# Kernel optimization log

Hardware: AMD Instinct MI355X
Metric: run time of the kernel (lower is better)

## Reference

```python
import jax, jax.numpy as jnp
import numpy as np

B, N, S, D = 8, 8192, 4, 256


def setup_inputs() -> dict:
    key = jax.random.key(0)
    kx, kj, kk, k1, k2, k3, k4 = jax.random.split(key, 7)
    x = jax.random.normal(kx, (B, N, D), dtype=jnp.float32)
    ji = jax.random.randint(kj, (B, N, S), 0, N, dtype=jnp.int64)
    ki = jax.random.randint(kk, (B, N, S), 0, N, dtype=jnp.int64)
    # params of nn.Sequential(Linear(3D, D), GELU, Linear(D, D))
    W1 = jax.random.normal(k1, (3 * D, D), dtype=jnp.float32) * 0.02
    b1 = jax.random.normal(k2, (D,), dtype=jnp.float32) * 0.02
    W2 = jax.random.normal(k3, (D, D), dtype=jnp.float32) * 0.02
    b2 = jax.random.normal(k4, (D,), dtype=jnp.float32) * 0.02
    return {"x": x, "ji": ji, "ki": ki, "W1": W1, "b1": b1, "W2": W2, "b2": b2}


def reference(x, ji, ki, W1, b1, W2, b2):
    # gather neighbor features per batch element: [B,N,S,D]
    gather = jax.vmap(lambda xb, ib: xb[ib])
    xj = gather(x, ji)
    xk = gather(x, ki)
    xi = jnp.broadcast_to(x[:, :, None, :], (B, N, S, D))
    h = jnp.concatenate([xi, xj, xk], axis=-1)            # [B,N,S,3D]
    h = jax.nn.gelu(jnp.einsum('bnse,ed->bnsd', h, W1) + b1, approximate=False)
    out = jnp.einsum('bnse,ed->bnsd', h, W2) + b2         # [B,N,S,D]
    return out.mean(axis=2)                               # [B,N,D]
```

## Files before the change

### kernel.cpp

```cpp
#include <hip/hip_runtime.h>
#include <hip/hip_bf16.h>

#define Bb 8
#define Nn 8192
#define Ss 4
#define Dd 256
#define MTOT (Bb*Nn)

typedef unsigned short u16;
typedef short short8 __attribute__((ext_vector_type(8)));
typedef unsigned short u16x4 __attribute__((ext_vector_type(4)));
typedef float f32x4 __attribute__((ext_vector_type(4)));

static __device__ __forceinline__ float bf2f(u16 v) {
  union { unsigned int u; float f; } x; x.u = ((unsigned int)v) << 16; return x.f;
}
static __device__ __forceinline__ u16 f2bf(float f) {
  union { float f; unsigned int u; } x; x.f = f;
  unsigned int u = x.u;
  return (u16)((u + 0x7fffu + ((u >> 16) & 1u)) >> 16);
}

static __device__ __forceinline__ float gelu_fast(float x) {
  float x2 = x * x;
  float z = x * (-2.3021277f - 0.10294456f * x2);
  float e = __builtin_amdgcn_exp2f(z);
  return x * __builtin_amdgcn_rcpf(1.0f + e);
}

__global__ __launch_bounds__(256) void prep_kernel(
    const float* __restrict__ x, const float* __restrict__ W1,
    const float* __restrict__ W2,
    u16* __restrict__ xb, u16* __restrict__ W1t, u16* __restrict__ W2t)
{
  int bid = blockIdx.x, t = threadIdx.x;
  if (bid < 16384) {
    size_t i = ((size_t)bid * 256 + t) * 4;
    f32x4 v = *(const f32x4*)&x[i];
    u16x4 o;
    o[0] = f2bf(v[0]); o[1] = f2bf(v[1]); o[2] = f2bf(v[2]); o[3] = f2bf(v[3]);
    *(u16x4*)&xb[i] = o;
  } else if (bid < 16384 + 768) {
    int j = (bid - 16384) * 256 + t;
    int n = j >> 8, k = j & 255;
    int tb = n >> 8, d = n & 255;
    W1t[j] = f2bf(W1[(size_t)(tb * 256 + k) * 256 + d]);
  } else {
    int j = (bid - 17152) * 256 + t;
    int n = j >> 8, k = j & 255;
    W2t[j] = f2bf(W2[(size_t)k * 256 + n]);
  }
}

template<int MODE>
__global__ __launch_bounds__(256) void gemm128(
    const u16* __restrict__ Ag, const u16* __restrict__ Btg,
    void* __restrict__ Outv, const float* __restrict__ bias, int ldOut)
{
  __shared__ u16 As[128 * 64];
  __shared__ u16 Bs[128 * 64];
  const int t = threadIdx.x;
  const int w = t >> 6, lane = t & 63;
  const int wm = (w >> 1) * 64, wn = (w & 1) * 64;
  const int lr = lane & 15;
  const int lk = (lane >> 4) * 8;
  const size_t m0 = (size_t)blockIdx.x * 128;
  const int n0 = blockIdx.y * 128;

  f32x4 acc[4][4];
#pragma unroll
  for (int m = 0; m < 4; ++m)
#pragma unroll
    for (int n = 0; n < 4; ++n)
      acc[m][n] = (f32x4){0.f, 0.f, 0.f, 0.f};

  for (int kt = 0; kt < 4; ++kt) {
#pragma unroll
    for (int pass = 0; pass < 4; ++pass) {
      int c = pass * 256 + t;
      int row = c >> 3, cc = c & 7;
      const u16* ga = Ag + (m0 + row) * 256 + kt * 64 + cc * 8;
      u16* la = As + pass * 2048 + (t & 192) * 8;
      __builtin_amdgcn_global_load_lds(
          (const __attribute__((address_space(1))) void*)ga,
          (__attribute__((address_space(3))) void*)la, 16, 0, 0);
      const u16* gb = Btg + (size_t)(n0 + row) * 256 + kt * 64 + cc * 8;
      u16* lb = Bs + pass * 2048 + (t & 192) * 8;
      __builtin_amdgcn_global_load_lds(
          (const __attribute__((address_space(1))) void*)gb,
          (__attribute__((address_space(3))) void*)lb, 16, 0, 0);
    }
    __syncthreads();
#pragma unroll
    for (int kk = 0; kk < 2; ++kk) {
      short8 af[4], bfr[4];
#pragma unroll
      for (int m = 0; m < 4; ++m)
        af[m] = *(const short8*)&As[(wm + m * 16 + lr) * 64 + kk * 32 + lk];
#pragma unroll
      for (int n = 0; n < 4; ++n)
        bfr[n] = *(const short8*)&Bs[(wn + n * 16 + lr) * 64 + kk * 32 + lk];
#pragma unroll
      for (int m = 0; m < 4; ++m)
#pragma unroll
        for (int n = 0; n < 4; ++n)
          acc[m][n] = __builtin_amdgcn_mfma_f32_16x16x32_bf16(
              af[m], bfr[n], acc[m][n], 0, 0, 0);
    }
    __syncthreads();
  }

#pragma unroll
  for (int m = 0; m < 4; ++m) {
    int rbase = wm + m * 16 + ((lane >> 4) << 2);
#pragma unroll
    for (int n = 0; n < 4; ++n) {
      int col = n0 + wn + n * 16 + (lane & 15);
#pragma unroll
      for (int rr = 0; rr < 4; ++rr) {
        size_t row = m0 + rbase + rr;
        if (MODE == 0) {
          ((u16*)Outv)[row * (size_t)ldOut + col] = f2bf(acc[m][n][rr]);
        } else {
          ((float*)Outv)[row * (size_t)ldOut + col] = acc[m][n][rr] + bias[col];
        }
      }
    }
  }
}

__global__ __launch_bounds__(256) void gather_gelu_mean(
    const u16* __restrict__ ABC, const int* __restrict__ ji,
    const int* __restrict__ ki, const float* __restrict__ b1,
    u16* __restrict__ Hm)
{
  int t = threadIdx.x, w = t >> 6, lane = t & 63;
  size_t r = (size_t)blockIdx.x * 4 + w;
  int base = ((int)(r >> 13)) << 13;
  int d0 = lane * 4;

  f32x4 bias = *(const f32x4*)&b1[d0];
  u16x4 av = *(const u16x4*)(ABC + r * 768 + d0);
  float a0 = bf2f(av[0]) + bias[0];
  float a1 = bf2f(av[1]) + bias[1];
  float a2 = bf2f(av[2]) + bias[2];
  float a3 = bf2f(av[3]) + bias[3];

  const int* jr = ji + r * 4;
  const int* kr = ki + r * 4;
  float acc0 = 0.f, acc1 = 0.f, acc2 = 0.f, acc3 = 0.f;
#pragma unroll
  for (int s = 0; s < 4; ++s) {
    size_t gj = (size_t)(base + jr[s]);
    size_t gk = (size_t)(base + kr[s]);
    u16x4 bv = *(const u16x4*)(ABC + gj * 768 + 256 + d0);
    u16x4 cv = *(const u16x4*)(ABC + gk * 768 + 512 + d0);
    float x0 = a0 + bf2f(bv[0]) + bf2f(cv[0]);
    float x1 = a1 + bf2f(bv[1]) + bf2f(cv[1]);
    float x2 = a2 + bf2f(bv[2]) + bf2f(cv[2]);
    float x3 = a3 + bf2f(bv[3]) + bf2f(cv[3]);
    acc0 += gelu_fast(x0);
    acc1 += gelu_fast(x1);
    acc2 += gelu_fast(x2);
    acc3 += gelu_fast(x3);
  }
  u16x4 hv;
  hv[0] = f2bf(acc0 * 0.25f);
  hv[1] = f2bf(acc1 * 0.25f);
  hv[2] = f2bf(acc2 * 0.25f);
  hv[3] = f2bf(acc3 * 0.25f);
  *(u16x4*)(Hm + r * 256 + d0) = hv;
}

extern "C" void kernel_launch(void* const* d_in, const int* in_sizes, int n_in,
                              void* d_out, int out_size, void* d_ws, size_t ws_size,
                              hipStream_t stream) {
  (void)in_sizes; (void)n_in; (void)out_size; (void)ws_size;
  const float* x  = (const float*)d_in[0];
  const int*   ji = (const int*)d_in[1];
  const int*   ki = (const int*)d_in[2];
  const float* W1 = (const float*)d_in[3];
  const float* b1 = (const float*)d_in[4];
  const float* W2 = (const float*)d_in[5];
  const float* b2 = (const float*)d_in[6];
  float* out = (float*)d_out;

  char* ws = (char*)d_ws;
  u16* xb  = (u16*)ws;  ws += (size_t)MTOT * 256 * 2;
  u16* ABC = (u16*)ws;  ws += (size_t)MTOT * 768 * 2;
  u16* Hm  = (u16*)ws;  ws += (size_t)MTOT * 256 * 2;
  u16* W1t = (u16*)ws;  ws += 768 * 256 * 2;
  u16* W2t = (u16*)ws;  ws += 256 * 256 * 2;

  prep_kernel<<<17408, 256, 0, stream>>>(x, W1, W2, xb, W1t, W2t);

  dim3 g1(MTOT / 128, 768 / 128);
  gemm128<0><<<g1, 256, 0, stream>>>(xb, W1t, (void*)ABC, nullptr, 768);

  gather_gelu_mean<<<MTOT / 4, 256, 0, stream>>>(ABC, ji, ki, b1, Hm);

  dim3 g2(MTOT / 128, 256 / 128);
  gemm128<1><<<g2, 256, 0, stream>>>(Hm, W2t, (void*)out, b2, 256);
}
```

Baseline: 137.5 us.

## Swizzle LDS tiles with XOR and remap GEMM blocks across XCDs

Applies an XOR swizzle to the 16-byte chunk index when staging A and B tiles into LDS via global_load_lds, with a matching XOR on the fragment reads, to remove bank conflicts from row-strided MFMA operand loads. It also flattens the GEMM grid to 1D and remaps block IDs so consecutive blocks on the same XCD share M rows, improving L2 reuse of A tiles across N blocks. This adds index arithmetic and assumes the grid size is a multiple of 8.

```diff
diff --git a/kernel.cpp b/kernel.cpp
--- a/kernel.cpp
+++ b/kernel.cpp
@@ -52,7 +52,7 @@
   }
 }
 
-template<int MODE>
+template<int MODE, int NBLK>
 __global__ __launch_bounds__(256) void gemm128(
     const u16* __restrict__ Ag, const u16* __restrict__ Btg,
     void* __restrict__ Outv, const float* __restrict__ bias, int ldOut)
@@ -64,8 +64,12 @@
   const int wm = (w >> 1) * 64, wn = (w & 1) * 64;
   const int lr = lane & 15;
   const int lk = (lane >> 4) * 8;
-  const size_t m0 = (size_t)blockIdx.x * 128;
-  const int n0 = blockIdx.y * 128;
+
+  const int cpx = gridDim.x >> 3;
+  const int bid = blockIdx.x;
+  const int swz = (bid & 7) * cpx + (bid >> 3);
+  const int n0 = (swz % NBLK) * 128;
+  const size_t m0 = (size_t)(swz / NBLK) * 128;
 
   f32x4 acc[4][4];
 #pragma unroll
@@ -79,12 +83,13 @@
     for (int pass = 0; pass < 4; ++pass) {
       int c = pass * 256 + t;
       int row = c >> 3, cc = c & 7;
-      const u16* ga = Ag + (m0 + row) * 256 + kt * 64 + cc * 8;
+      int scc = cc ^ (row & 7);
+      const u16* ga = Ag + (m0 + row) * 256 + kt * 64 + scc * 8;
       u16* la = As + pass * 2048 + (t & 192) * 8;
       __builtin_amdgcn_global_load_lds(
           (const __attribute__((address_space(1))) void*)ga,
           (__attribute__((address_space(3))) void*)la, 16, 0, 0);
-      const u16* gb = Btg + (size_t)(n0 + row) * 256 + kt * 64 + cc * 8;
+      const u16* gb = Btg + (size_t)(n0 + row) * 256 + kt * 64 + scc * 8;
       u16* lb = Bs + pass * 2048 + (t & 192) * 8;
       __builtin_amdgcn_global_load_lds(
           (const __attribute__((address_space(1))) void*)gb,
@@ -95,11 +100,15 @@
     for (int kk = 0; kk < 2; ++kk) {
       short8 af[4], bfr[4];
 #pragma unroll
-      for (int m = 0; m < 4; ++m)
-        af[m] = *(const short8*)&As[(wm + m * 16 + lr) * 64 + kk * 32 + lk];
-#pragma unroll
-      for (int n = 0; n < 4; ++n)
-        bfr[n] = *(const short8*)&Bs[(wn + n * 16 + lr) * 64 + kk * 32 + lk];
+      for (int m = 0; m < 4; ++m) {
+        int rA = wm + m * 16 + lr;
+        af[m] = *(const short8*)&As[(rA * 64 + kk * 32 + lk) ^ ((rA & 7) << 3)];
+      }
+#pragma unroll
+      for (int n = 0; n < 4; ++n) {
+        int rB = wn + n * 16 + lr;
+        bfr[n] = *(const short8*)&Bs[(rB * 64 + kk * 32 + lk) ^ ((rB & 7) << 3)];
+      }
 #pragma unroll
       for (int m = 0; m < 4; ++m)
 #pragma unroll
@@ -194,11 +203,11 @@
 
   prep_kernel<<<17408, 256, 0, stream>>>(x, W1, W2, xb, W1t, W2t);
 
-  dim3 g1(MTOT / 128, 768 / 128);
-  gemm128<0><<<g1, 256, 0, stream>>>(xb, W1t, (void*)ABC, nullptr, 768);
+  gemm128<0, 6><<<(MTOT / 128) * 6, 256, 0, stream>>>(
+      xb, W1t, (void*)ABC, nullptr, 768);
 
   gather_gelu_mean<<<MTOT / 4, 256, 0, stream>>>(ABC, ji, ki, b1, Hm);
 
-  dim3 g2(MTOT / 128, 256 / 128);
-  gemm128<1><<<g2, 256, 0, stream>>>(Hm, W2t, (void*)out, b2, 256);
-}
+  gemm128<1, 2><<<(MTOT / 128) * 2, 256, 0, stream>>>(
+      Hm, W2t, (void*)out, b2, 256);
+}
```

After: 122.3 us. -11.1%, faster.
